# Optimization experiments

Measured on AMD Instinct MI355X. Metric: run time of the kernel, lower is better.

The kernel has to match this reference:

```python
import jax, jax.numpy as jnp
import numpy as np
import math

SIZE = (60, 270, 480)           # full video T, H, W
CHANNELS = 14                   # sum of per-level grid channels 8+4+2
GRID_SIZES = [(60, 16, 16, 8), (30, 8, 8, 4), (15, 4, 4, 2)]
IDX_MAX = (60, 3, 5)            # patch grid -> patch_size (1, 90, 96)
PADDING = (0, 1, 1)
N_PATCH = 64
MANIP_LBASE = 2.0
MANIP_LEVELS = 8
INIT_SCALE = 1e-3


def setup_inputs() -> dict:
    key = jax.random.key(0)
    kt, kh, kw = jax.random.split(key, 3)
    idx = jnp.stack([
        jax.random.randint(kt, (N_PATCH,), 0, IDX_MAX[0]),
        jax.random.randint(kh, (N_PATCH,), 0, IDX_MAX[1]),
        jax.random.randint(kw, (N_PATCH,), 0, IDX_MAX[2]),
    ], axis=1).astype(jnp.int32)
    inp = {
        "idx": idx,
        "idx_max": jnp.asarray(IDX_MAX, dtype=jnp.int32),
        "padding": jnp.asarray(PADDING, dtype=jnp.int32),
    }
    for i, (T, H, W, C) in enumerate(GRID_SIZES):
        k = jax.random.fold_in(key, 10 + i)
        inp[f"grid{i}"] = jax.random.normal(k, (T * H * W, C), jnp.float32) * INIT_SCALE
    return inp


def _pixel_idx_1d(ix, size_d, nmax_d, pad_d):
    # ix: [N] patch index along one dim -> ([N, P+2*pad] clipped pixel idx, mask)
    p = size_d // nmax_d
    offs = jnp.arange(-pad_d, p + pad_d)
    raw = ix[:, None] * p + offs[None, :]
    mask = ((raw >= 0) & (raw < size_d)).astype(jnp.float32)
    return jnp.clip(raw, 0, size_d - 1), mask


def reference(idx, idx_max, padding, grid0, grid1, grid2):
    T, H, W = SIZE
    im = tuple(int(v) for v in np.asarray(idx_max))
    pad = tuple(int(v) for v in np.asarray(padding))
    patch = tuple(SIZE[d] // im[d] for d in range(3))
    ppad = tuple(patch[d] + 2 * pad[d] for d in range(3))

    # Multi-level grids -> trilinear upsample to full (T,H,W,C_i), concat on C.
    # jax.image.resize 'trilinear' uses half-pixel centers == torch align_corners=False.
    enc_splits = []
    for g, (Tg, Hg, Wg, Cg) in zip((grid0, grid1, grid2), GRID_SIZES):
        enc_splits.append(jax.image.resize(g.reshape(Tg, Hg, Wg, Cg), (T, H, W, Cg), method="trilinear"))
    enc = jnp.concatenate(enc_splits, axis=-1).reshape(T * H * W, CHANNELS)

    it, mt = _pixel_idx_1d(idx[:, 0], T, im[0], pad[0])
    ih, mh = _pixel_idx_1d(idx[:, 1], H, im[1], pad[1])
    iw, mw = _pixel_idx_1d(idx[:, 2], W, im[2], pad[2])

    flat = (it[:, :, None, None] * (H * W) + ih[:, None, :, None] * W + iw[:, None, None, :]).reshape(-1)
    mask = (mt[:, :, None, None] * mh[:, None, :, None] * mw[:, None, None, :]).reshape(-1, 1)

    t_embed = (mask * enc[flat]).reshape((idx.shape[0],) + ppad + (CHANNELS,))

    bases = (MANIP_LBASE ** jnp.arange(MANIP_LEVELS, dtype=jnp.float32)) * math.pi
    v = idx[:, 0].astype(jnp.float32)[:, None] * bases
    t_manip = jnp.concatenate([jnp.sin(v), jnp.cos(v)], axis=-1)  # [N, 2*levels]

    return t_embed, t_manip
```

## Files before the change

### kernel.cpp

```cpp
#include <hip/hip_runtime.h>
#include <math.h>


#define N_PATCH 64
#define PPAD_H 92
#define PPAD_W 98
#define CH 14
#define PIX_PER_PATCH (PPAD_H * PPAD_W)
#define ROWS_PER_BLOCK 2
#define BLOCKS_PER_PATCH 46
#define PX_PER_BLOCK 196
#define F4_PER_BLOCK (PX_PER_BLOCK * CH / 4)
#define ELEMS_PER_PATCH (PIX_PER_PATCH * CH)
#define ELEMS_PER_BLOCK (PX_PER_BLOCK * CH)
#define TOTAL_EMBED (N_PATCH * ELEMS_PER_PATCH)
#define TOTAL_MANIP (N_PATCH * 16)

#define RB_STRIDE 72
#define L1_OFF 48
#define L2_OFF 64

__device__ __forceinline__ float lerpf(float a, float b, float f) {
    return a + f * (b - a);
}

__device__ __forceinline__ int wcell0(int rw0, float sw, int Wg) {
    float x = ((float)rw0 + 0.5f) * sw - 0.5f;
    int w0 = (int)floorf(x);
    return min(max(w0, 0), Wg - 1);
}

__global__ __launch_bounds__(256) void embed_kernel(
    const int* __restrict__ idx,
    const float* __restrict__ g0,
    const float* __restrict__ g1,
    const float* __restrict__ g2,
    float* __restrict__ out)
{
    __shared__ __align__(16) float s_V[ROWS_PER_BLOCK * RB_STRIDE];
    __shared__ float4 s_wl[3][PPAD_W];
    __shared__ __align__(16) float s_buf[PX_PER_BLOCK * CH];

    const int tid = threadIdx.x;
    const int bx  = blockIdx.x;
    const int n   = blockIdx.y;
    const int it  = idx[3 * n + 0];
    const int ih  = idx[3 * n + 1];
    const int iw  = idx[3 * n + 2];
    const int rw0 = iw * 96 - 1;

    const float sw0 = (float)((double)16 / 480.0);
    const float sw1 = (float)((double)8  / 480.0);
    const float sw2 = (float)((double)4  / 480.0);
    const float sh0 = (float)((double)16 / 270.0);
    const float sh1 = (float)((double)8  / 270.0);
    const float sh2 = (float)((double)4  / 270.0);

    if (bx == 0 && n == 0) {
        float* om = out + TOTAL_EMBED;
        for (int e = tid; e < TOTAL_MANIP; e += 256) {
            int nn = e >> 4;
            int j  = e & 15;
            int l  = j & 7;
            float base = (float)M_PI * (float)(1 << l);
            float v = (float)idx[3 * nn + 0] * base;
            double dv = (double)v;
            om[e] = (float)((j < 8) ? sin(dv) : cos(dv));
        }
    }

    if (tid < 96) {
        int chn  = tid & 7;
        int u    = tid >> 3;
        int row  = (u >= 6);
        int cell = u - 6 * row;
        int rh   = ih * 90 + (bx * 2 + row) - 1;
        float mh = ((unsigned)rh < 270u) ? 1.0f : 0.0f;
        float xh = ((float)rh + 0.5f) * sh0 - 0.5f;
        float ff = floorf(xh);
        float fh = xh - ff;
        int h0 = (int)ff;
        int h0c = min(max(h0, 0), 15), h1c = min(h0 + 1, 15);
        int cw = min(wcell0(rw0, sw0, 16) + cell, 15);
        const float* base = g0 + (size_t)it * 2048;
        float a = base[(h0c * 16 + cw) * 8 + chn];
        float b = base[(h1c * 16 + cw) * 8 + chn];
        s_V[row * RB_STRIDE + cell * 8 + chn] = mh * lerpf(a, b, fh);
    } else if (tid < 128) {
        int i    = tid - 96;
        int chn  = i & 3;
        int u    = i >> 2;
        int row  = (u >= 4);
        int cell = u - 4 * row;
        int rh   = ih * 90 + (bx * 2 + row) - 1;
        float mh = ((unsigned)rh < 270u) ? 1.0f : 0.0f;
        float xh = ((float)rh + 0.5f) * sh1 - 0.5f;
        float ff = floorf(xh);
        float fh = xh - ff;
        int h0 = (int)ff;
        int h0c = min(max(h0, 0), 7), h1c = min(h0 + 1, 7);
        float xt = ((float)it + 0.5f) * 0.5f - 0.5f;
        float ftf = floorf(xt);
        float ft  = xt - ftf;
        int t0 = (int)ftf;
        int t0c = min(max(t0, 0), 29), t1c = min(t0 + 1, 29);
        int cw = min(wcell0(rw0, sw1, 8) + cell, 7);
        float a00 = g1[((t0c * 8 + h0c) * 8 + cw) * 4 + chn];
        float a01 = g1[((t0c * 8 + h1c) * 8 + cw) * 4 + chn];
        float a10 = g1[((t1c * 8 + h0c) * 8 + cw) * 4 + chn];
        float a11 = g1[((t1c * 8 + h1c) * 8 + cw) * 4 + chn];
        s_V[row * RB_STRIDE + L1_OFF + cell * 4 + chn] =
            mh * lerpf(lerpf(a00, a01, fh), lerpf(a10, a11, fh), ft);
    } else if (tid < 140) {
        int i    = tid - 128;
        int chn  = i & 1;
        int u    = i >> 1;
        int row  = (u >= 3);
        int cell = u - 3 * row;
        int rh   = ih * 90 + (bx * 2 + row) - 1;
        float mh = ((unsigned)rh < 270u) ? 1.0f : 0.0f;
        float xh = ((float)rh + 0.5f) * sh2 - 0.5f;
        float ff = floorf(xh);
        float fh = xh - ff;
        int h0 = (int)ff;
        int h0c = min(max(h0, 0), 3), h1c = min(h0 + 1, 3);
        float xt = ((float)it + 0.5f) * 0.25f - 0.5f;
        float ftf = floorf(xt);
        float ft  = xt - ftf;
        int t0 = (int)ftf;
        int t0c = min(max(t0, 0), 14), t1c = min(t0 + 1, 14);
        int cw = min(wcell0(rw0, sw2, 4) + cell, 3);
        float a00 = g2[((t0c * 4 + h0c) * 4 + cw) * 2 + chn];
        float a01 = g2[((t0c * 4 + h1c) * 4 + cw) * 2 + chn];
        float a10 = g2[((t1c * 4 + h0c) * 4 + cw) * 2 + chn];
        float a11 = g2[((t1c * 4 + h1c) * 4 + cw) * 2 + chn];
        s_V[row * RB_STRIDE + L2_OFF + cell * 2 + chn] =
            mh * lerpf(lerpf(a00, a01, fh), lerpf(a10, a11, fh), ft);
    }

    for (int i = tid; i < 3 * PPAD_W; i += 256) {
        int lvl = (i >= PPAD_W) + (i >= 2 * PPAD_W);
        int ww  = i - PPAD_W * lvl;
        int Wg  = (lvl == 0) ? 16 : ((lvl == 1) ? 8 : 4);
        int cs  = (lvl == 0) ? 8  : ((lvl == 1) ? 4 : 2);
        int bb  = (lvl == 0) ? 0  : ((lvl == 1) ? L1_OFF : L2_OFF);
        float sw = (lvl == 0) ? sw0 : ((lvl == 1) ? sw1 : sw2);
        int rw = iw * 96 + ww - 1;
        float mask = ((unsigned)rw < 480u) ? 1.0f : 0.0f;
        float x  = ((float)rw + 0.5f) * sw - 0.5f;
        float ff = floorf(x);
        float f  = x - ff;
        int w0 = (int)ff;
        int wa = min(max(w0, 0), Wg - 1);
        int wb = min(w0 + 1, Wg - 1);
        int C0 = wcell0(rw0, sw, Wg);
        s_wl[lvl][ww] = make_float4(__int_as_float(bb + (wa - C0) * cs),
                                    __int_as_float(bb + (wb - C0) * cs), f, mask);
    }

    __syncthreads();

    if (tid < PX_PER_BLOCK) {
        int row = (tid >= PPAD_W);
        int ww  = tid - PPAD_W * row;
        const float* V = s_V + row * RB_STRIDE;
        float r[CH];

        float4 wl0 = s_wl[0][ww];
        {
            int oA = __float_as_int(wl0.x), oB = __float_as_int(wl0.y);
            float fw = wl0.z;
            float4 A0 = *(const float4*)(V + oA);
            float4 A1 = *(const float4*)(V + oA + 4);
            float4 B0 = *(const float4*)(V + oB);
            float4 B1 = *(const float4*)(V + oB + 4);
            r[0] = lerpf(A0.x, B0.x, fw);
            r[1] = lerpf(A0.y, B0.y, fw);
            r[2] = lerpf(A0.z, B0.z, fw);
            r[3] = lerpf(A0.w, B0.w, fw);
            r[4] = lerpf(A1.x, B1.x, fw);
            r[5] = lerpf(A1.y, B1.y, fw);
            r[6] = lerpf(A1.z, B1.z, fw);
            r[7] = lerpf(A1.w, B1.w, fw);
        }
        {
            float4 wl1 = s_wl[1][ww];
            int oA = __float_as_int(wl1.x), oB = __float_as_int(wl1.y);
            float fw = wl1.z;
            float4 A = *(const float4*)(V + oA);
            float4 B = *(const float4*)(V + oB);
            r[8]  = lerpf(A.x, B.x, fw);
            r[9]  = lerpf(A.y, B.y, fw);
            r[10] = lerpf(A.z, B.z, fw);
            r[11] = lerpf(A.w, B.w, fw);
        }
        {
            float4 wl2 = s_wl[2][ww];
            int oA = __float_as_int(wl2.x), oB = __float_as_int(wl2.y);
            float fw = wl2.z;
            float2 A = *(const float2*)(V + oA);
            float2 B = *(const float2*)(V + oB);
            r[12] = lerpf(A.x, B.x, fw);
            r[13] = lerpf(A.y, B.y, fw);
        }
        float mw = wl0.w;
        float2* b = (float2*)(s_buf + tid * CH);
        b[0] = make_float2(mw * r[0],  mw * r[1]);
        b[1] = make_float2(mw * r[2],  mw * r[3]);
        b[2] = make_float2(mw * r[4],  mw * r[5]);
        b[3] = make_float2(mw * r[6],  mw * r[7]);
        b[4] = make_float2(mw * r[8],  mw * r[9]);
        b[5] = make_float2(mw * r[10], mw * r[11]);
        b[6] = make_float2(mw * r[12], mw * r[13]);
    }
    __syncthreads();

    const float4* sb = (const float4*)s_buf;
    float4* gb = (float4*)(out + (size_t)n * ELEMS_PER_PATCH + bx * ELEMS_PER_BLOCK);
    for (int j = tid; j < F4_PER_BLOCK; j += 256) gb[j] = sb[j];
}

extern "C" void kernel_launch(void* const* d_in, const int* in_sizes, int n_in,
                              void* d_out, int out_size, void* d_ws, size_t ws_size,
                              hipStream_t stream) {
    const int*   idx = (const int*)  d_in[0];
    const float* g0  = (const float*)d_in[3];
    const float* g1  = (const float*)d_in[4];
    const float* g2  = (const float*)d_in[5];
    float* out = (float*)d_out;

    dim3 grid(BLOCKS_PER_PATCH, N_PATCH);
    embed_kernel<<<grid, 256, 0, stream>>>(idx, g0, g1, g2, out);
}
```

Measured before the change: 12.76 us.

## Process twelve rows per block with double-buffered shared staging of output chunks

Each block now covers 12 rows of a patch instead of 2, so there are 8 blocks per patch instead of 46. The per-row vertical interpolation values are computed for all 12 rows in a strided loop, and the horizontal weight table is built once per block. Output is produced in 2-row chunks through two alternating shared buffers, so the global store of one chunk can overlap the compute of the next. The goal is to spread the setup cost over more rows and cut block count. The price is a much smaller grid (512 blocks), which lowers parallelism on a GPU with many CUs, plus a serial per-block loop.

```diff
diff --git a/kernel.cpp b/kernel.cpp
--- a/kernel.cpp
+++ b/kernel.cpp
@@ -7,18 +7,18 @@
 #define PPAD_W 98
 #define CH 14
 #define PIX_PER_PATCH (PPAD_H * PPAD_W)
-#define ROWS_PER_BLOCK 2
-#define BLOCKS_PER_PATCH 46
-#define PX_PER_BLOCK 196
-#define F4_PER_BLOCK (PX_PER_BLOCK * CH / 4)
+#define ROWS_PER_BLOCK 12
+#define BLOCKS_PER_PATCH 8
 #define ELEMS_PER_PATCH (PIX_PER_PATCH * CH)
-#define ELEMS_PER_BLOCK (PX_PER_BLOCK * CH)
+#define ELEMS_PER_ROW (PPAD_W * CH)
+#define F4_PER_CHUNK (2 * ELEMS_PER_ROW / 4)
 #define TOTAL_EMBED (N_PATCH * ELEMS_PER_PATCH)
 #define TOTAL_MANIP (N_PATCH * 16)
 
 #define RB_STRIDE 72
 #define L1_OFF 48
 #define L2_OFF 64
+#define V_ENTRIES (ROWS_PER_BLOCK * 70)
 
 __device__ __forceinline__ float lerpf(float a, float b, float f) {
     return a + f * (b - a);
@@ -39,7 +39,8 @@
 {
     __shared__ __align__(16) float s_V[ROWS_PER_BLOCK * RB_STRIDE];
     __shared__ float4 s_wl[3][PPAD_W];
-    __shared__ __align__(16) float s_buf[PX_PER_BLOCK * CH];
+    __shared__ __align__(16) float s_bufA[2 * ELEMS_PER_ROW];
+    __shared__ __align__(16) float s_bufB[2 * ELEMS_PER_ROW];
 
     const int tid = threadIdx.x;
     const int bx  = blockIdx.x;
@@ -48,6 +49,7 @@
     const int ih  = idx[3 * n + 1];
     const int iw  = idx[3 * n + 2];
     const int rw0 = iw * 96 - 1;
+    const int row0 = bx * ROWS_PER_BLOCK;
 
     const float sw0 = (float)((double)16 / 480.0);
     const float sw1 = (float)((double)8  / 480.0);
@@ -69,73 +71,67 @@
         }
     }
 
-    if (tid < 96) {
-        int chn  = tid & 7;
-        int u    = tid >> 3;
-        int row  = (u >= 6);
-        int cell = u - 6 * row;
-        int rh   = ih * 90 + (bx * 2 + row) - 1;
+    const int C0_0 = wcell0(rw0, sw0, 16);
+    const int C0_1 = wcell0(rw0, sw1, 8);
+    const int C0_2 = wcell0(rw0, sw2, 4);
+    for (int e = tid; e < V_ENTRIES; e += 256) {
+        int row = e / 70;
+        int off = e - 70 * row;
+        int rh  = ih * 90 + row0 + row - 1;
         float mh = ((unsigned)rh < 270u) ? 1.0f : 0.0f;
-        float xh = ((float)rh + 0.5f) * sh0 - 0.5f;
-        float ff = floorf(xh);
-        float fh = xh - ff;
-        int h0 = (int)ff;
-        int h0c = min(max(h0, 0), 15), h1c = min(h0 + 1, 15);
-        int cw = min(wcell0(rw0, sw0, 16) + cell, 15);
-        const float* base = g0 + (size_t)it * 2048;
-        float a = base[(h0c * 16 + cw) * 8 + chn];
-        float b = base[(h1c * 16 + cw) * 8 + chn];
-        s_V[row * RB_STRIDE + cell * 8 + chn] = mh * lerpf(a, b, fh);
-    } else if (tid < 128) {
-        int i    = tid - 96;
-        int chn  = i & 3;
-        int u    = i >> 2;
-        int row  = (u >= 4);
-        int cell = u - 4 * row;
-        int rh   = ih * 90 + (bx * 2 + row) - 1;
-        float mh = ((unsigned)rh < 270u) ? 1.0f : 0.0f;
-        float xh = ((float)rh + 0.5f) * sh1 - 0.5f;
-        float ff = floorf(xh);
-        float fh = xh - ff;
-        int h0 = (int)ff;
-        int h0c = min(max(h0, 0), 7), h1c = min(h0 + 1, 7);
-        float xt = ((float)it + 0.5f) * 0.5f - 0.5f;
-        float ftf = floorf(xt);
-        float ft  = xt - ftf;
-        int t0 = (int)ftf;
-        int t0c = min(max(t0, 0), 29), t1c = min(t0 + 1, 29);
-        int cw = min(wcell0(rw0, sw1, 8) + cell, 7);
-        float a00 = g1[((t0c * 8 + h0c) * 8 + cw) * 4 + chn];
-        float a01 = g1[((t0c * 8 + h1c) * 8 + cw) * 4 + chn];
-        float a10 = g1[((t1c * 8 + h0c) * 8 + cw) * 4 + chn];
-        float a11 = g1[((t1c * 8 + h1c) * 8 + cw) * 4 + chn];
-        s_V[row * RB_STRIDE + L1_OFF + cell * 4 + chn] =
-            mh * lerpf(lerpf(a00, a01, fh), lerpf(a10, a11, fh), ft);
-    } else if (tid < 140) {
-        int i    = tid - 128;
-        int chn  = i & 1;
-        int u    = i >> 1;
-        int row  = (u >= 3);
-        int cell = u - 3 * row;
-        int rh   = ih * 90 + (bx * 2 + row) - 1;
-        float mh = ((unsigned)rh < 270u) ? 1.0f : 0.0f;
-        float xh = ((float)rh + 0.5f) * sh2 - 0.5f;
-        float ff = floorf(xh);
-        float fh = xh - ff;
-        int h0 = (int)ff;
-        int h0c = min(max(h0, 0), 3), h1c = min(h0 + 1, 3);
-        float xt = ((float)it + 0.5f) * 0.25f - 0.5f;
-        float ftf = floorf(xt);
-        float ft  = xt - ftf;
-        int t0 = (int)ftf;
-        int t0c = min(max(t0, 0), 14), t1c = min(t0 + 1, 14);
-        int cw = min(wcell0(rw0, sw2, 4) + cell, 3);
-        float a00 = g2[((t0c * 4 + h0c) * 4 + cw) * 2 + chn];
-        float a01 = g2[((t0c * 4 + h1c) * 4 + cw) * 2 + chn];
-        float a10 = g2[((t1c * 4 + h0c) * 4 + cw) * 2 + chn];
-        float a11 = g2[((t1c * 4 + h1c) * 4 + cw) * 2 + chn];
-        s_V[row * RB_STRIDE + L2_OFF + cell * 2 + chn] =
-            mh * lerpf(lerpf(a00, a01, fh), lerpf(a10, a11, fh), ft);
+        float v;
+        if (off < L1_OFF) {
+            int cell = off >> 3, chn = off & 7;
+            float xh = ((float)rh + 0.5f) * sh0 - 0.5f;
+            float ff = floorf(xh);
+            float fh = xh - ff;
+            int h0 = (int)ff;
+            int h0c = min(max(h0, 0), 15), h1c = min(h0 + 1, 15);
+            int cw = min(C0_0 + cell, 15);
+            const float* base = g0 + (size_t)it * 2048;
+            float a = base[(h0c * 16 + cw) * 8 + chn];
+            float b = base[(h1c * 16 + cw) * 8 + chn];
+            v = mh * lerpf(a, b, fh);
+        } else if (off < L2_OFF) {
+            int o = off - L1_OFF;
+            int cell = o >> 2, chn = o & 3;
+            float xh = ((float)rh + 0.5f) * sh1 - 0.5f;
+            float ff = floorf(xh);
+            float fh = xh - ff;
+            int h0 = (int)ff;
+            int h0c = min(max(h0, 0), 7), h1c = min(h0 + 1, 7);
+            float xt = ((float)it + 0.5f) * 0.5f - 0.5f;
+            float ftf = floorf(xt);
+            float ft  = xt - ftf;
+            int t0 = (int)ftf;
+            int t0c = min(max(t0, 0), 29), t1c = min(t0 + 1, 29);
+            int cw = min(C0_1 + cell, 7);
+            float a00 = g1[((t0c * 8 + h0c) * 8 + cw) * 4 + chn];
+            float a01 = g1[((t0c * 8 + h1c) * 8 + cw) * 4 + chn];
+            float a10 = g1[((t1c * 8 + h0c) * 8 + cw) * 4 + chn];
+            float a11 = g1[((t1c * 8 + h1c) * 8 + cw) * 4 + chn];
+            v = mh * lerpf(lerpf(a00, a01, fh), lerpf(a10, a11, fh), ft);
+        } else {
+            int o = off - L2_OFF;
+            int cell = o >> 1, chn = o & 1;
+            float xh = ((float)rh + 0.5f) * sh2 - 0.5f;
+            float ff = floorf(xh);
+            float fh = xh - ff;
+            int h0 = (int)ff;
+            int h0c = min(max(h0, 0), 3), h1c = min(h0 + 1, 3);
+            float xt = ((float)it + 0.5f) * 0.25f - 0.5f;
+            float ftf = floorf(xt);
+            float ft  = xt - ftf;
+            int t0 = (int)ftf;
+            int t0c = min(max(t0, 0), 14), t1c = min(t0 + 1, 14);
+            int cw = min(C0_2 + cell, 3);
+            float a00 = g2[((t0c * 4 + h0c) * 4 + cw) * 2 + chn];
+            float a01 = g2[((t0c * 4 + h1c) * 4 + cw) * 2 + chn];
+            float a10 = g2[((t1c * 4 + h0c) * 4 + cw) * 2 + chn];
+            float a11 = g2[((t1c * 4 + h1c) * 4 + cw) * 2 + chn];
+            v = mh * lerpf(lerpf(a00, a01, fh), lerpf(a10, a11, fh), ft);
+        }
+        s_V[row * RB_STRIDE + off] = v;
     }
 
     for (int i = tid; i < 3 * PPAD_W; i += 256) {
@@ -144,6 +140,7 @@
         int Wg  = (lvl == 0) ? 16 : ((lvl == 1) ? 8 : 4);
         int cs  = (lvl == 0) ? 8  : ((lvl == 1) ? 4 : 2);
         int bb  = (lvl == 0) ? 0  : ((lvl == 1) ? L1_OFF : L2_OFF);
+        int C0  = (lvl == 0) ? C0_0 : ((lvl == 1) ? C0_1 : C0_2);
         float sw = (lvl == 0) ? sw0 : ((lvl == 1) ? sw1 : sw2);
         int rw = iw * 96 + ww - 1;
         float mask = ((unsigned)rw < 480u) ? 1.0f : 0.0f;
@@ -153,71 +150,83 @@
         int w0 = (int)ff;
         int wa = min(max(w0, 0), Wg - 1);
         int wb = min(w0 + 1, Wg - 1);
-        int C0 = wcell0(rw0, sw, Wg);
         s_wl[lvl][ww] = make_float4(__int_as_float(bb + (wa - C0) * cs),
                                     __int_as_float(bb + (wb - C0) * cs), f, mask);
     }
 
     __syncthreads();
 
-    if (tid < PX_PER_BLOCK) {
-        int row = (tid >= PPAD_W);
-        int ww  = tid - PPAD_W * row;
-        const float* V = s_V + row * RB_STRIDE;
-        float r[CH];
-
+    const bool active = tid < 2 * PPAD_W;
+    int par = 0, oA0 = 0, oB0 = 0, oA1 = 0, oB1 = 0, oA2 = 0, oB2 = 0;
+    float fw0 = 0.f, fw1 = 0.f, fw2 = 0.f, mw = 0.f;
+    if (active) {
+        par = tid >= PPAD_W;
+        int ww = tid - PPAD_W * par;
         float4 wl0 = s_wl[0][ww];
-        {
-            int oA = __float_as_int(wl0.x), oB = __float_as_int(wl0.y);
-            float fw = wl0.z;
-            float4 A0 = *(const float4*)(V + oA);
-            float4 A1 = *(const float4*)(V + oA + 4);
-            float4 B0 = *(const float4*)(V + oB);
-            float4 B1 = *(const float4*)(V + oB + 4);
-            r[0] = lerpf(A0.x, B0.x, fw);
-            r[1] = lerpf(A0.y, B0.y, fw);
-            r[2] = lerpf(A0.z, B0.z, fw);
-            r[3] = lerpf(A0.w, B0.w, fw);
-            r[4] = lerpf(A1.x, B1.x, fw);
-            r[5] = lerpf(A1.y, B1.y, fw);
-            r[6] = lerpf(A1.z, B1.z, fw);
-            r[7] = lerpf(A1.w, B1.w, fw);
-        }
-        {
-            float4 wl1 = s_wl[1][ww];
-            int oA = __float_as_int(wl1.x), oB = __float_as_int(wl1.y);
-            float fw = wl1.z;
-            float4 A = *(const float4*)(V + oA);
-            float4 B = *(const float4*)(V + oB);
-            r[8]  = lerpf(A.x, B.x, fw);
-            r[9]  = lerpf(A.y, B.y, fw);
-            r[10] = lerpf(A.z, B.z, fw);
-            r[11] = lerpf(A.w, B.w, fw);
-        }
-        {
-            float4 wl2 = s_wl[2][ww];
-            int oA = __float_as_int(wl2.x), oB = __float_as_int(wl2.y);
-            float fw = wl2.z;
-            float2 A = *(const float2*)(V + oA);
-            float2 B = *(const float2*)(V + oB);
-            r[12] = lerpf(A.x, B.x, fw);
-            r[13] = lerpf(A.y, B.y, fw);
-        }
-        float mw = wl0.w;
-        float2* b = (float2*)(s_buf + tid * CH);
-        b[0] = make_float2(mw * r[0],  mw * r[1]);
-        b[1] = make_float2(mw * r[2],  mw * r[3]);
-        b[2] = make_float2(mw * r[4],  mw * r[5]);
-        b[3] = make_float2(mw * r[6],  mw * r[7]);
-        b[4] = make_float2(mw * r[8],  mw * r[9]);
-        b[5] = make_float2(mw * r[10], mw * r[11]);
-        b[6] = make_float2(mw * r[12], mw * r[13]);
-    }
+        float4 wl1 = s_wl[1][ww];
+        float4 wl2 = s_wl[2][ww];
+        oA0 = __float_as_int(wl0.x); oB0 = __float_as_int(wl0.y); fw0 = wl0.z;
+        oA1 = __float_as_int(wl1.x); oB1 = __float_as_int(wl1.y); fw1 = wl1.z;
+        oA2 = __float_as_int(wl2.x); oB2 = __float_as_int(wl2.y); fw2 = wl2.z;
+        mw  = wl0.w;
+    }
+
+    const int nrows   = min(ROWS_PER_BLOCK, PPAD_H - row0);
+    const int nchunks = nrows >> 1;
+    float* outp = out + (size_t)n * ELEMS_PER_PATCH;
+
+    auto compute_chunk = [&](int c, float* __restrict__ buf) {
+        if (!active) return;
+        const float* V = s_V + (2 * c + par) * RB_STRIDE;
+        float4 A0 = *(const float4*)(V + oA0);
+        float4 A1 = *(const float4*)(V + oA0 + 4);
+        float4 B0 = *(const float4*)(V + oB0);
+        float4 B1 = *(const float4*)(V + oB0 + 4);
+        float4 C1a = *(const float4*)(V + oA1);
+        float4 C1b = *(const float4*)(V + oB1);
+        float2 C2a = *(const float2*)(V + oA2);
+        float2 C2b = *(const float2*)(V + oB2);
+        float r0  = mw * lerpf(A0.x, B0.x, fw0);
+        float r1  = mw * lerpf(A0.y, B0.y, fw0);
+        float r2  = mw * lerpf(A0.z, B0.z, fw0);
+        float r3  = mw * lerpf(A0.w, B0.w, fw0);
+        float r4  = mw * lerpf(A1.x, B1.x, fw0);
+        float r5  = mw * lerpf(A1.y, B1.y, fw0);
+        float r6  = mw * lerpf(A1.z, B1.z, fw0);
+        float r7  = mw * lerpf(A1.w, B1.w, fw0);
+        float r8  = mw * lerpf(C1a.x, C1b.x, fw1);
+        float r9  = mw * lerpf(C1a.y, C1b.y, fw1);
+        float r10 = mw * lerpf(C1a.z, C1b.z, fw1);
+        float r11 = mw * lerpf(C1a.w, C1b.w, fw1);
+        float r12 = mw * lerpf(C2a.x, C2b.x, fw2);
+        float r13 = mw * lerpf(C2a.y, C2b.y, fw2);
+        float2* b = (float2*)(buf + tid * CH);
+        b[0] = make_float2(r0,  r1);
+        b[1] = make_float2(r2,  r3);
+        b[2] = make_float2(r4,  r5);
+        b[3] = make_float2(r6,  r7);
+        b[4] = make_float2(r8,  r9);
+        b[5] = make_float2(r10, r11);
+        b[6] = make_float2(r12, r13);
+    };
+
+    compute_chunk(0, s_bufA);
     __syncthreads();
-
-    const float4* sb = (const float4*)s_buf;
-    float4* gb = (float4*)(out + (size_t)n * ELEMS_PER_PATCH + bx * ELEMS_PER_BLOCK);
-    for (int j = tid; j < F4_PER_BLOCK; j += 256) gb[j] = sb[j];
+    for (int c = 1; c < nchunks; ++c) {
+        float* prev = (c & 1) ? s_bufA : s_bufB;
+        float* cur  = (c & 1) ? s_bufB : s_bufA;
+        const float4* sb = (const float4*)prev;
+        float4* gb = (float4*)(outp + (size_t)(row0 + 2 * (c - 1)) * ELEMS_PER_ROW);
+        for (int j = tid; j < F4_PER_CHUNK; j += 256) gb[j] = sb[j];
+        compute_chunk(c, cur);
+        __syncthreads();
+    }
+    {
+        float* last = ((nchunks - 1) & 1) ? s_bufB : s_bufA;
+        const float4* sb = (const float4*)last;
+        float4* gb = (float4*)(outp + (size_t)(row0 + 2 * (nchunks - 1)) * ELEMS_PER_ROW);
+        for (int j = tid; j < F4_PER_CHUNK; j += 256) gb[j] = sb[j];
+    }
 }
 
 extern "C" void kernel_launch(void* const* d_in, const int* in_sizes, int n_in,
```

Measured after the change: 15.02 us. +17.7%, slower.
